# Kernel tuning notes

Measured on AMD Instinct MI355X. Metric: run time of the kernel, lower is better.

The kernel has to match this reference:

```python
import jax, jax.numpy as jnp
import numpy as np

B, L, E, H = 4, 4096, 1024, 16
D = E // H  # head_dim = 64
EPS = 1e-4


def setup_inputs() -> dict:
    key = jax.random.key(0)
    k1, k2, k3 = jax.random.split(key, 3)
    x = jax.random.normal(k1, (B, L, E), dtype=jnp.float32)
    W_qkv = jax.random.normal(k2, (E, 3 * E), dtype=jnp.float32) * (1.0 / np.sqrt(E))
    b_qkv = jnp.zeros((3 * E,), dtype=jnp.float32)
    W_out = jax.random.normal(k3, (E, E), dtype=jnp.float32) * (1.0 / np.sqrt(E))
    b_out = jnp.zeros((E,), dtype=jnp.float32)
    return {"x": x, "W_qkv": W_qkv, "b_qkv": b_qkv, "W_out": W_out, "b_out": b_out}


def reference(x, W_qkv, b_qkv, W_out, b_out):
    Bb, Ll, Ee = x.shape
    qkv = x @ W_qkv + b_qkv                      # [B, L, 3E]
    q, k, v = jnp.split(qkv, 3, axis=-1)
    # [B, H, L, D]
    q = q.reshape(Bb, Ll, H, D).transpose(0, 2, 1, 3)
    k = k.reshape(Bb, Ll, H, D).transpose(0, 2, 1, 3)
    v = v.reshape(Bb, Ll, H, D).transpose(0, 2, 1, 3)

    positions = jnp.arange(Ll, dtype=jnp.float32).reshape(1, 1, Ll, 1)
    cos_w = jnp.cos(jnp.pi / 2 * positions / Ll)
    sin_w = jnp.sin(jnp.pi / 2 * positions / Ll)

    q_prime = jax.nn.relu(q)
    k_prime = jax.nn.relu(k)

    q_cos, q_sin = q_prime * cos_w, q_prime * sin_w
    k_cos, k_sin = k_prime * cos_w, k_prime * sin_w

    # O(L) linear attention: accumulate KV outer products per head
    kv_cos = jnp.einsum('bhld,bhle->bhde', k_cos, v)      # [B,H,D,D]
    kv_sin = jnp.einsum('bhld,bhle->bhde', k_sin, v)
    context = (jnp.einsum('bhld,bhde->bhle', q_cos, kv_cos)
               + jnp.einsum('bhld,bhde->bhle', q_sin, kv_sin))  # [B,H,L,D]

    k_cos_sum = k_cos.sum(axis=2)                          # [B,H,D]
    k_sin_sum = k_sin.sum(axis=2)
    norm = (jnp.einsum('bhld,bhd->bhl', q_cos, k_cos_sum)
            + jnp.einsum('bhld,bhd->bhl', q_sin, k_sin_sum))

    output = context / (norm[..., None] + EPS)
    output = output.transpose(0, 2, 1, 3).reshape(Bb, Ll, Ee)
    return output @ W_out + b_out
```

## Files before the change

kernel.cpp:

```cpp
#include <hip/hip_runtime.h>
#include <hip/hip_bf16.h>
#include <cstdint>
#include <cstddef>

#define BB 4
#define LL 4096
#define HH 16
#define M1 16384
#define E3 3072
#define EE 1024
#define ANGC 3.8349519697141029e-4f
#define EPSC 1e-4f

typedef __attribute__((ext_vector_type(8))) short bf16x8;
typedef __attribute__((ext_vector_type(4))) float f32x4;
typedef __attribute__((ext_vector_type(16))) float f32x16;
typedef __attribute__((ext_vector_type(8))) unsigned short us8;

static __device__ __forceinline__ float bf2f(unsigned short u) {
  union { unsigned int i; float f; } a; a.i = ((unsigned int)u) << 16; return a.f;
}
static __device__ __forceinline__ unsigned short f2bf(float x) {
  union { float f; unsigned int i; } a; a.f = x;
  unsigned int r = a.i + 0x7FFFu + ((a.i >> 16) & 1u);
  return (unsigned short)(r >> 16);
}
static __device__ __forceinline__ void gload16(const void* g, void* l) {
  __builtin_amdgcn_global_load_lds((const __attribute__((address_space(1))) void*)g,
                                   (__attribute__((address_space(3))) void*)l, 16, 0, 0);
}

#define BAR()   asm volatile("s_barrier" ::: "memory")
#define VMC4()  asm volatile("s_waitcnt vmcnt(4)" ::: "memory")
#define VMC0()  asm volatile("s_waitcnt vmcnt(0)" ::: "memory")
#define PRIO1() __builtin_amdgcn_s_setprio(1)
#define PRIO0() __builtin_amdgcn_s_setprio(0)

static __device__ __forceinline__ void transpose_body(const float* __restrict__ src,
                                                      unsigned short* __restrict__ dst,
                                                      int R, int C, int bx, int by,
                                                      float (*tile)[33]) {
  int c0 = bx * 32, r0 = by * 32;
  int tx = threadIdx.x & 31, ty = threadIdx.x >> 5;
#pragma unroll
  for (int k = 0; k < 4; ++k)
    tile[ty + 8*k][tx] = src[(size_t)(r0 + ty + 8*k) * C + c0 + tx];
  __syncthreads();
#pragma unroll
  for (int k = 0; k < 4; ++k)
    dst[(size_t)(c0 + ty + 8*k) * R + r0 + tx] = f2bf(tile[tx][ty + 8*k]);
}

__global__ __launch_bounds__(256) void k_prep(const float* __restrict__ x,
                                              const float* __restrict__ Wq,
                                              const float* __restrict__ Wo,
                                              unsigned short* __restrict__ xb,
                                              unsigned short* __restrict__ WqT,
                                              unsigned short* __restrict__ WoT) {
  __shared__ float tile[32][33];
  const int bid = blockIdx.x;
  if (bid < 8192) {
    int i = bid * 256 + threadIdx.x;
    const float4* s = (const float4*)x + (size_t)i * 2;
    float4 a = s[0], b = s[1];
    us8 o;
    o[0]=f2bf(a.x); o[1]=f2bf(a.y); o[2]=f2bf(a.z); o[3]=f2bf(a.w);
    o[4]=f2bf(b.x); o[5]=f2bf(b.y); o[6]=f2bf(b.z); o[7]=f2bf(b.w);
    *(us8*)(xb + (size_t)i * 8) = o;
  } else if (bid < 8192 + 3072) {
    int r = bid - 8192;
    transpose_body(Wq, WqT, 1024, 3072, r % 96, r / 96, tile);
  } else {
    int r = bid - 11264;
    transpose_body(Wo, WoT, 1024, 1024, r % 32, r / 32, tile);
  }
}


static __device__ __forceinline__ bf16x8 rdfrag(const char* base, int row, int ck) {
  return *(const bf16x8*)(base + row * 128 + (((ck) ^ ((row) & 7)) << 4));
}

static __device__ __forceinline__ void stage2h(const unsigned short* __restrict__ base,
                                               size_t off, size_t rowK64, char* ldst) {
  gload16(base + off, ldst);
  gload16(base + off + rowK64, ldst + 8192);
}

#define PH_B(BbP)                                                               \
  do {                                                                          \
    _Pragma("unroll")                                                           \
    for (int nb = 0; nb < 2; ++nb)                                              \
      _Pragma("unroll")                                                         \
      for (int kk = 0; kk < 4; ++kk)                                            \
        bK[nb][kk] = rdfrag((BbP), wc * 64 + nb * 32 + l31, kk * 2 + l5);       \
  } while (0)

#define PH_A32(AbP, mb, AR)                                                     \
  do {                                                                          \
    _Pragma("unroll")                                                           \
    for (int kk = 0; kk < 4; ++kk)                                              \
      AR[kk] = rdfrag((AbP), wr * 128 + (mb) * 32 + l31, kk * 2 + l5);          \
  } while (0)

#define MMA8(mb, AR)                                                            \
  do {                                                                          \
    _Pragma("unroll")                                                           \
    for (int kk = 0; kk < 4; ++kk) {                                            \
      acc[(mb)][0] = __builtin_amdgcn_mfma_f32_32x32x16_bf16(                   \
          AR[kk], bK[0][kk], acc[(mb)][0], 0, 0, 0);                            \
      acc[(mb)][1] = __builtin_amdgcn_mfma_f32_32x32x16_bf16(                   \
          AR[kk], bK[1][kk], acc[(mb)][1], 0, 0, 0);                            \
    }                                                                           \
  } while (0)

template<int MODE>
__global__ __launch_bounds__(512, 1) void k_gemm256(const unsigned short* __restrict__ A,
                                                    const unsigned short* __restrict__ Bt,
                                                    const float* __restrict__ bias,
                                                    void* __restrict__ Cout,
                                                    int N, int K) {
  __shared__ __align__(16) unsigned short lds[4][16384];
  const int tid = threadIdx.x;
  const int wid = tid >> 6, lane = tid & 63;
  const int l31 = lane & 31, l5 = lane >> 5;
  const int wr = wid >> 2, wc = wid & 3;

  const int nx = gridDim.x;
  const int rawbid = blockIdx.y * nx + blockIdx.x;
  const int xcd = rawbid & 7, s = rawbid >> 3;
  const int g = s >> 5, r = s & 31;
  const int bm = (xcd * 8 + (r & 7)) * 256;
  const int bn = (g * 4 + (r >> 3)) * 256;

  char* LA0 = (char*)&lds[0][0];
  char* LB0 = (char*)&lds[1][0];
  char* LA1 = (char*)&lds[2][0];
  char* LB1 = (char*)&lds[3][0];

  f32x16 acc[4][2] = {};
  bf16x8 bK[2][4], aP[4], aQ[4];

  const int rr = tid >> 3, cc = tid & 7;
  const size_t rowK64 = (size_t)64 * K, rowK128 = (size_t)128 * K;
  const size_t aoff = (size_t)(bm + rr) * K + ((cc ^ (rr & 7)) << 3);
  const size_t boff = (size_t)(bn + rr) * K + ((cc ^ (rr & 7)) << 3);

#define STAGE_A(h, kt, L) stage2h(A,  aoff + (h) * rowK128 + (kt), rowK64, (L) + (h) * 16384 + tid * 16)
#define STAGE_B(h, kt, L) stage2h(Bt, boff + (h) * rowK128 + (kt), rowK64, (L) + (h) * 16384 + tid * 16)

  const int NT = K >> 6, NI = NT >> 1;

  STAGE_A(0, 0, LA0); STAGE_A(1, 0, LA0);
  STAGE_B(0, 0, LB0); STAGE_B(1, 0, LB0);
  STAGE_B(0, 64, LB1); STAGE_B(1, 64, LB1);
  VMC4();
  BAR();

  for (int it = 0; it < NI; ++it) {
    const int kt1 = (2*it + 1) << 6;
    const int kt2 = (2*it + 2) << 6;
    const int kt3 = (2*it + 3) << 6;
    const bool s2 = kt2 < K, s3 = kt3 < K;

    PH_B(LB0); PH_A32(LA0, 0, aP);
    STAGE_A(0, kt1, LA1);
    BAR(); PRIO1(); MMA8(0, aP); PRIO0();

    PH_A32(LA0, 1, aQ);
    STAGE_A(1, kt1, LA1);
    BAR(); PRIO1(); MMA8(1, aQ); PRIO0();

    PH_A32(LA0, 2, aP);
    if (s2) STAGE_B(0, kt2, LB0);
    BAR(); PRIO1(); MMA8(2, aP); PRIO0();

    PH_A32(LA0, 3, aQ);
    if (s2) STAGE_B(1, kt2, LB0);
    BAR(); PRIO1(); MMA8(3, aQ); PRIO0();
    if (it == NI - 1) { VMC0(); } else { VMC4(); }
    BAR();

    PH_B(LB1); PH_A32(LA1, 0, aP);
    if (s2) STAGE_A(0, kt2, LA0);
    BAR(); PRIO1(); MMA8(0, aP); PRIO0();

    PH_A32(LA1, 1, aQ);
    if (s2) STAGE_A(1, kt2, LA0);
    BAR(); PRIO1(); MMA8(1, aQ); PRIO0();

    PH_A32(LA1, 2, aP);
    if (s3) STAGE_B(0, kt3, LB1);
    BAR(); PRIO1(); MMA8(2, aP); PRIO0();

    PH_A32(LA1, 3, aQ);
    if (s3) STAGE_B(1, kt3, LB1);
    BAR(); PRIO1(); MMA8(3, aQ); PRIO0();
    VMC4();
    BAR();
  }
#undef STAGE_A
#undef STAGE_B

  {
    float* strip = (float*)((char*)&lds[0][0] + wid * 16384);
    float bias_v[2]; bool relu_v[2];
#pragma unroll
    for (int nb = 0; nb < 2; ++nb) {
      int col = bn + wc*64 + nb*32 + l31;
      bias_v[nb] = bias[col];
      relu_v[nb] = (MODE == 0) && (col < 2048);
    }
#pragma unroll
    for (int mb = 0; mb < 4; ++mb) {
#pragma unroll
      for (int nb = 0; nb < 2; ++nb)
#pragma unroll
        for (int j = 0; j < 16; ++j) {
          float v = acc[mb][nb][j] + bias_v[nb];
          if (relu_v[nb]) v = fmaxf(v, 0.0f);
          int row = (j & 3) + 8*(j >> 2) + 4*l5;
          strip[row*68 + nb*32 + l31] = v;
        }
#pragma unroll
      for (int itr = 0; itr < 8; ++itr) {
        int ch = itr*64 + lane;
        int row = ch >> 4, cg = ch & 15;
        float4 v = *(const float4*)(strip + row*68 + cg*4);
        size_t base = (size_t)(bm + wr*128 + mb*32 + row) * N + bn + wc*64 + cg*4;
        if (MODE == 0) {
          ushort4 o;
          o.x = f2bf(v.x); o.y = f2bf(v.y); o.z = f2bf(v.z); o.w = f2bf(v.w);
          *(ushort4*)((unsigned short*)Cout + base) = o;
        } else {
          *(float4*)((float*)Cout + base) = v;
        }
      }
    }
  }
}

__global__ __launch_bounds__(256) void k_stage2(const unsigned short* __restrict__ qkv,
                                                float* __restrict__ kvb,
                                                float* __restrict__ ksumb) {
  __shared__ __align__(16) unsigned short kcT[4096];
  __shared__ __align__(16) unsigned short ksT[4096];
  __shared__ __align__(16) unsigned short vT [4096];
  const int tid = threadIdx.x;
  const int head = blockIdx.y;
  const int b = head >> 4, h = head & 15;
  const int lane = tid & 63, wid = tid >> 6;
  const int lr = lane & 15, lg = lane >> 4;
  const int mt = wid >> 1, eh = wid & 1;
  const int lp = tid & 31;
  const int piece = tid >> 5;

  f32x4 acc[2][4] = {};
  float ksacc = 0.0f;
  const int mtk = tid >> 6, dk = tid & 63;
  const size_t qbase = (size_t)b * LL * E3;

  for (int sc = 0; sc < 4; ++sc) {
    const int lbase = blockIdx.x * 256 + sc * 64;
    __syncthreads();
    {
      const int l0 = 2 * lp;
      const int p0 = lbase + l0;
      float s0, c0, s1, c1;
      __sincosf((float)p0 * ANGC, &s0, &c0);
      __sincosf((float)(p0 + 1) * ANGC, &s1, &c1);
      const unsigned short* kp = qkv + qbase + (size_t)p0 * E3 + 1024 + h*64 + piece*8;
      us8 kr0 = *(const us8*)kp;
      us8 kr1 = *(const us8*)(kp + E3);
      us8 vr0 = *(const us8*)(kp + 1024);
      us8 vr1 = *(const us8*)(kp + 1024 + E3);
#pragma unroll
      for (int i = 0; i < 8; ++i) {
        int d = piece*8 + i;
        float ka = bf2f(kr0[i]), kb = bf2f(kr1[i]);
        unsigned int kcp = (unsigned int)f2bf(c0*ka) | ((unsigned int)f2bf(c1*kb) << 16);
        unsigned int ksp = (unsigned int)f2bf(s0*ka) | ((unsigned int)f2bf(s1*kb) << 16);
        unsigned int vp  = (unsigned int)vr0[i] | ((unsigned int)vr1[i] << 16);
        int off = d*128 + ((((l0 >> 3) ^ (d & 7))) << 4) + (l0 & 7) * 2;
        *(unsigned int*)((char*)kcT + off) = kcp;
        *(unsigned int*)((char*)ksT + off) = ksp;
        *(unsigned int*)((char*)vT  + off) = vp;
      }
    }
    __syncthreads();
    if (tid < 128) {
      const unsigned short* basep = mtk ? ksT : kcT;
      float sum = 0.0f;
#pragma unroll
      for (int cch = 0; cch < 8; ++cch) {
        us8 r2 = *(const us8*)((const char*)basep + dk*128 + ((cch ^ (dk & 7)) << 4));
#pragma unroll
        for (int i = 0; i < 8; ++i) sum += bf2f(r2[i]);
      }
      ksacc += sum;
    }
    {
      const unsigned short* kT = mt ? ksT : kcT;
      bf16x8 af[2][2], bf[2][4];
#pragma unroll
      for (int kk = 0; kk < 2; ++kk) {
#pragma unroll
        for (int m = 0; m < 2; ++m) {
          int e = eh*32 + m*16 + lr;
          af[kk][m] = *(const bf16x8*)((const char*)vT + e*128 + ((((kk*4)+lg) ^ (e & 7)) << 4));
        }
#pragma unroll
        for (int n = 0; n < 4; ++n) {
          int d = n*16 + lr;
          bf[kk][n] = *(const bf16x8*)((const char*)kT + d*128 + ((((kk*4)+lg) ^ (d & 7)) << 4));
        }
      }
#pragma unroll
      for (int kk = 0; kk < 2; ++kk)
#pragma unroll
        for (int m = 0; m < 2; ++m)
#pragma unroll
          for (int n = 0; n < 4; ++n)
            acc[m][n] = __builtin_amdgcn_mfma_f32_16x16x32_bf16(af[kk][m], bf[kk][n], acc[m][n], 0, 0, 0);
    }
  }
  float* dst = kvb + (size_t)head * 8192 + mt * 4096;
#pragma unroll
  for (int m = 0; m < 2; ++m)
#pragma unroll
    for (int n = 0; n < 4; ++n)
#pragma unroll
      for (int j = 0; j < 4; ++j) {
        int e = eh*32 + m*16 + lg*4 + j;
        int d = n*16 + lr;
        atomicAdd(&dst[e*64 + d], acc[m][n][j]);
      }
  if (tid < 128) atomicAdd(&ksumb[head*128 + mtk*64 + dk], ksacc);
}

__global__ __launch_bounds__(256) void k_stage3(const unsigned short* __restrict__ qkv,
                                                const float* __restrict__ kvb,
                                                const float* __restrict__ ksumb,
                                                unsigned short* __restrict__ att) {
  __shared__ __align__(16) unsigned short Bl[144 * 64];
  const int tid = threadIdx.x;
  const int head = blockIdx.y;
  const int b = head >> 4, h = head & 15;
  const int l0 = blockIdx.x * 128;
  const int lane = tid & 63, w = tid >> 6;
  const int lr = lane & 15, lg = lane >> 4;

  {
    int c = tid >> 1, half = tid & 1;
    const float* src = kvb + (size_t)head * 8192 + (c >> 6) * 4096 + (c & 63) * 64 + half * 32;
    float fv[32];
#pragma unroll
    for (int q = 0; q < 8; ++q) *(float4*)(fv + q*4) = *(const float4*)(src + q*4);
#pragma unroll
    for (int q2 = 0; q2 < 4; ++q2) {
      us8 o;
#pragma unroll
      for (int i = 0; i < 8; ++i) o[i] = f2bf(fv[q2*8 + i]);
      int chunk = half*4 + q2;
      *(us8*)((char*)Bl + c*128 + ((chunk ^ (c & 7)) << 4)) = o;
    }
    if (tid < 16) {
      int cc = 128 + (tid >> 3), q = tid & 7;
      const float* s2 = ksumb + head*128 + (tid >> 3)*64 + q*8;
      us8 o;
#pragma unroll
      for (int i = 0; i < 8; ++i) o[i] = f2bf(s2[i]);
      *(us8*)((char*)Bl + cc*128 + ((q ^ (cc & 7)) << 4)) = o;
    } else if (tid < 128) {
      int idx = tid - 16;
      int cc = 130 + (idx >> 3), q = idx & 7;
      us8 o = {0,0,0,0,0,0,0,0};
      *(us8*)((char*)Bl + cc*128 + ((q ^ (cc & 7)) << 4)) = o;
    }
  }
  __syncthreads();

  f32x4 acc[2][9] = {};
  bf16x8 af[2][2];
  const size_t qrow0 = (size_t)(b * LL + l0 + w * 32);
#pragma unroll
  for (int kk = 0; kk < 2; ++kk)
#pragma unroll
    for (int m = 0; m < 2; ++m)
      af[m][kk] = *(const bf16x8*)(qkv + (qrow0 + m*16 + lr) * E3 + h*64 + kk*32 + lg*8);
#pragma unroll
  for (int kk = 0; kk < 2; ++kk)
#pragma unroll
    for (int n = 0; n < 9; ++n) {
      int cc = n*16 + lr;
      bf16x8 bb = *(const bf16x8*)((const char*)Bl + cc*128 + ((((kk*4)+lg) ^ (cc & 7)) << 4));
#pragma unroll
      for (int m = 0; m < 2; ++m)
        acc[m][n] = __builtin_amdgcn_mfma_f32_16x16x32_bf16(af[m][kk], bb, acc[m][n], 0, 0, 0);
    }

  __syncthreads();
  unsigned short* strip = (unsigned short*)Bl + w * 2048;
#pragma unroll
  for (int m = 0; m < 2; ++m)
#pragma unroll
    for (int j = 0; j < 4; ++j) {
      int rloc = m*16 + lg*4 + j;
      int pos = l0 + w*32 + rloc;
      float s_, c_;
      __sincosf((float)pos * ANGC, &s_, &c_);
      float nc = __shfl(acc[m][8][j], lane & 48, 64);
      float ns = __shfl(acc[m][8][j], (lane & 48) | 1, 64);
      float rn = 1.0f / (c_ * nc + s_ * ns + EPSC);
#pragma unroll
      for (int n = 0; n < 4; ++n) {
        float ctx = (c_ * acc[m][n][j] + s_ * acc[m][n+4][j]) * rn;
        strip[rloc*64 + n*16 + lr] = f2bf(ctx);
      }
    }
  __syncthreads();
#pragma unroll
  for (int p = 0; p < 4; ++p) {
    int ch = p*64 + lane;
    int row = ch >> 3, piece = ch & 7;
    us8 o = *(const us8*)(strip + row*64 + piece*8);
    *(us8*)(att + (size_t)(b*LL + l0 + w*32 + row) * EE + h*64 + piece*8) = o;
  }
}

extern "C" void kernel_launch(void* const* d_in, const int* in_sizes, int n_in,
                              void* d_out, int out_size, void* d_ws, size_t ws_size,
                              hipStream_t stream) {
  const float* x     = (const float*)d_in[0];
  const float* W_qkv = (const float*)d_in[1];
  const float* b_qkv = (const float*)d_in[2];
  const float* W_out = (const float*)d_in[3];
  const float* b_out = (const float*)d_in[4];

  char* w = (char*)d_ws;
  unsigned short* xb  = (unsigned short*)(w);
  unsigned short* qkv = (unsigned short*)(w + 33554432);
  unsigned short* WqT = (unsigned short*)(w + 134217728);
  unsigned short* WoT = (unsigned short*)(w + 140509184);
  float* kvb   = (float*)(w + 142606336);
  float* ksum  = (float*)(w + 144703488);
  unsigned short* att = xb;

  hipMemsetAsync(kvb, 0, 2097152 + 32768, stream);
  k_prep<<<12288, 256, 0, stream>>>(x, W_qkv, W_out, xb, WqT, WoT);
  k_gemm256<0><<<dim3(12, 64), 512, 0, stream>>>(xb, WqT, b_qkv, (void*)qkv, 3072, 1024);
  k_stage2<<<dim3(16, 64), 256, 0, stream>>>(qkv, kvb, ksum);
  k_stage3<<<dim3(32, 64), 256, 0, stream>>>(qkv, kvb, ksum, att);
  k_gemm256<1><<<dim3(4, 64), 512, 0, stream>>>(att, WoT, b_out, d_out, 1024, 1024);
}
```

Baseline: 236.7 us.

## Switch GEMM LDS tiles to column-chunk-major layout and reswizzle stage2 transposes

The GEMM's LDS staging moves from row-major tiles with an XOR swizzle to a chunk-major layout, where each 16-byte K-chunk for all rows is contiguous. Each thread now loads one row's two K-chunks 32 elements apart, and fragment reads become simple strided row*16 accesses. The aim is to remove LDS bank conflicts and address arithmetic on the MFMA operand reads. The stage2 kernel also remaps threads so consecutive threads handle feature columns and adds a second-level swizzle (d&7)^(d>>3), aimed at cutting bank conflicts on the transposed LDS writes. Global load coalescing may change, since consecutive threads now read different rows.

```diff
diff --git a/kernel.cpp b/kernel.cpp
--- a/kernel.cpp
+++ b/kernel.cpp
@@ -77,14 +77,14 @@
 }
 
 
-static __device__ __forceinline__ bf16x8 rdfrag(const char* base, int row, int ck) {
-  return *(const bf16x8*)(base + row * 128 + (((ck) ^ ((row) & 7)) << 4));
-}
-
-static __device__ __forceinline__ void stage2h(const unsigned short* __restrict__ base,
-                                               size_t off, size_t rowK64, char* ldst) {
-  gload16(base + off, ldst);
-  gload16(base + off + rowK64, ldst + 8192);
+static __device__ __forceinline__ bf16x8 rdfrag32(const char* base, int row, int ck) {
+  return *(const bf16x8*)(base + ck * 4096 + row * 16);
+}
+
+static __device__ __forceinline__ void stageH(const unsigned short* __restrict__ M,
+                                              size_t off, char* ldst) {
+  gload16(M + off, ldst);
+  gload16(M + off + 32, ldst + 16384);
 }
 
 #define PH_B(BbP)                                                               \
@@ -93,14 +93,14 @@
     for (int nb = 0; nb < 2; ++nb)                                              \
       _Pragma("unroll")                                                         \
       for (int kk = 0; kk < 4; ++kk)                                            \
-        bK[nb][kk] = rdfrag((BbP), wc * 64 + nb * 32 + l31, kk * 2 + l5);       \
+        bK[nb][kk] = rdfrag32((BbP), wc * 64 + nb * 32 + l31, kk * 2 + l5);     \
   } while (0)
 
 #define PH_A32(AbP, mb, AR)                                                     \
   do {                                                                          \
     _Pragma("unroll")                                                           \
     for (int kk = 0; kk < 4; ++kk)                                              \
-      AR[kk] = rdfrag((AbP), wr * 128 + (mb) * 32 + l31, kk * 2 + l5);          \
+      AR[kk] = rdfrag32((AbP), wr * 128 + (mb) * 32 + l31, kk * 2 + l5);        \
   } while (0)
 
 #define MMA8(mb, AR)                                                            \
@@ -141,13 +141,14 @@
   f32x16 acc[4][2] = {};
   bf16x8 bK[2][4], aP[4], aQ[4];
 
-  const int rr = tid >> 3, cc = tid & 7;
-  const size_t rowK64 = (size_t)64 * K, rowK128 = (size_t)128 * K;
-  const size_t aoff = (size_t)(bm + rr) * K + ((cc ^ (rr & 7)) << 3);
-  const size_t boff = (size_t)(bn + rr) * K + ((cc ^ (rr & 7)) << 3);
-
-#define STAGE_A(h, kt, L) stage2h(A,  aoff + (h) * rowK128 + (kt), rowK64, (L) + (h) * 16384 + tid * 16)
-#define STAGE_B(h, kt, L) stage2h(Bt, boff + (h) * rowK128 + (kt), rowK64, (L) + (h) * 16384 + tid * 16)
+  const int rl = tid & 127, ck0 = tid >> 7;
+  const size_t rowK128 = (size_t)128 * K;
+  const size_t aoff = (size_t)(bm + rl) * K + ck0 * 8;
+  const size_t boff = (size_t)(bn + rl) * K + ck0 * 8;
+  const int dstoff = ck0 * 4096 + rl * 16;
+
+#define STAGE_A(h, kt, L) stageH(A,  aoff + (h) * rowK128 + (kt), (L) + dstoff + (h) * 2048)
+#define STAGE_B(h, kt, L) stageH(Bt, boff + (h) * rowK128 + (kt), (L) + dstoff + (h) * 2048)
 
   const int NT = K >> 6, NI = NT >> 1;
 
@@ -240,6 +241,8 @@
   }
 }
 
+static __device__ __forceinline__ int swz2(int d) { return (d & 7) ^ (d >> 3); }
+
 __global__ __launch_bounds__(256) void k_stage2(const unsigned short* __restrict__ qkv,
                                                 float* __restrict__ kvb,
                                                 float* __restrict__ ksumb) {
@@ -252,8 +255,8 @@
   const int lane = tid & 63, wid = tid >> 6;
   const int lr = lane & 15, lg = lane >> 4;
   const int mt = wid >> 1, eh = wid & 1;
-  const int lp = tid & 31;
-  const int piece = tid >> 5;
+  const int pr = tid >> 3;
+  const int pc = tid & 7;
 
   f32x4 acc[2][4] = {};
   float ksacc = 0.0f;
@@ -264,24 +267,25 @@
     const int lbase = blockIdx.x * 256 + sc * 64;
     __syncthreads();
     {
-      const int l0 = 2 * lp;
+      const int l0 = 2 * pr;
       const int p0 = lbase + l0;
       float s0, c0, s1, c1;
       __sincosf((float)p0 * ANGC, &s0, &c0);
       __sincosf((float)(p0 + 1) * ANGC, &s1, &c1);
-      const unsigned short* kp = qkv + qbase + (size_t)p0 * E3 + 1024 + h*64 + piece*8;
+      const unsigned short* kp = qkv + qbase + (size_t)p0 * E3 + 1024 + h*64 + pc*8;
       us8 kr0 = *(const us8*)kp;
       us8 kr1 = *(const us8*)(kp + E3);
       us8 vr0 = *(const us8*)(kp + 1024);
       us8 vr1 = *(const us8*)(kp + 1024 + E3);
+      const int cch = pr >> 2, wb = (pr & 3) * 4;
 #pragma unroll
       for (int i = 0; i < 8; ++i) {
-        int d = piece*8 + i;
+        int d = pc*8 + i;
         float ka = bf2f(kr0[i]), kb = bf2f(kr1[i]);
         unsigned int kcp = (unsigned int)f2bf(c0*ka) | ((unsigned int)f2bf(c1*kb) << 16);
         unsigned int ksp = (unsigned int)f2bf(s0*ka) | ((unsigned int)f2bf(s1*kb) << 16);
         unsigned int vp  = (unsigned int)vr0[i] | ((unsigned int)vr1[i] << 16);
-        int off = d*128 + ((((l0 >> 3) ^ (d & 7))) << 4) + (l0 & 7) * 2;
+        int off = d*128 + ((cch ^ swz2(d)) << 4) + wb;
         *(unsigned int*)((char*)kcT + off) = kcp;
         *(unsigned int*)((char*)ksT + off) = ksp;
         *(unsigned int*)((char*)vT  + off) = vp;
@@ -292,8 +296,8 @@
       const unsigned short* basep = mtk ? ksT : kcT;
       float sum = 0.0f;
 #pragma unroll
-      for (int cch = 0; cch < 8; ++cch) {
-        us8 r2 = *(const us8*)((const char*)basep + dk*128 + ((cch ^ (dk & 7)) << 4));
+      for (int cch2 = 0; cch2 < 8; ++cch2) {
+        us8 r2 = *(const us8*)((const char*)basep + dk*128 + ((cch2 ^ swz2(dk)) << 4));
 #pragma unroll
         for (int i = 0; i < 8; ++i) sum += bf2f(r2[i]);
       }
@@ -307,12 +311,12 @@
 #pragma unroll
         for (int m = 0; m < 2; ++m) {
           int e = eh*32 + m*16 + lr;
-          af[kk][m] = *(const bf16x8*)((const char*)vT + e*128 + ((((kk*4)+lg) ^ (e & 7)) << 4));
+          af[kk][m] = *(const bf16x8*)((const char*)vT + e*128 + ((((kk*4)+lg) ^ swz2(e)) << 4));
         }
 #pragma unroll
         for (int n = 0; n < 4; ++n) {
           int d = n*16 + lr;
-          bf[kk][n] = *(const bf16x8*)((const char*)kT + d*128 + ((((kk*4)+lg) ^ (d & 7)) << 4));
+          bf[kk][n] = *(const bf16x8*)((const char*)kT + d*128 + ((((kk*4)+lg) ^ swz2(d)) << 4));
         }
       }
 #pragma unroll
```

After: 254.4 us. +7.5%, slower.
